# Kernel tuning notes

Measured on AMD Instinct MI355X. Metric: run time of the kernel, lower is better.

## Reference

```python
import jax, jax.numpy as jnp
import numpy as np

NUM_HEADS = 32
HEAD_DIM = 128
NUM_KV_HEADS = 8
SCALE = 0.08838834764831845  # 1/sqrt(128)
T = 2048          # total packed tokens (total_q == total_k in delta branch)
N_SAL = 512       # number of salient rows
NUM_SEQS = 4
EPS = 1e-8
NEG = -1e30


def setup_inputs() -> dict:
    key = jax.random.key(0)
    ks = jax.random.split(key, 5)
    q = jax.random.normal(ks[0], (T, NUM_HEADS, HEAD_DIM), dtype=jnp.float32)
    k = jax.random.normal(ks[1], (T, NUM_KV_HEADS, HEAD_DIM), dtype=jnp.float32)
    v = jax.random.normal(ks[2], (N_SAL, NUM_KV_HEADS, HEAD_DIM), dtype=jnp.float32)
    v_cache = jax.random.normal(ks[3], (T, NUM_KV_HEADS, HEAD_DIM), dtype=jnp.float32)
    c_cache = jax.random.normal(ks[4], (T, NUM_HEADS * HEAD_DIM), dtype=jnp.float32)
    # unique, sorted salient row indices (torch index_copy requires well-defined scatter)
    idx_salient_row = (jnp.arange(N_SAL, dtype=jnp.int64) * (T // N_SAL))
    # 4 equal packed sequences
    cu_seqlens = jnp.array([0, 512, 1024, 1536, 2048], dtype=jnp.int64)
    return {"q": q, "k": k, "v": v, "v_cache": v_cache, "c_cache": c_cache,
            "idx_salient_row": idx_salient_row, "cu_seqlens": cu_seqlens}


def _segment_ids(cu_seqlens, n):
    # seg[i] = which packed sequence row i belongs to (searchsorted right on bounds)
    return jnp.searchsorted(cu_seqlens[1:], jnp.arange(n), side="right")


def _sdpa(q_, k_, v_, seg_q_, seg_k_):
    # GQA: repeat_interleave kv heads to match query heads
    n_rep = q_.shape[1] // k_.shape[1]
    if n_rep > 1:
        k_ = jnp.repeat(k_, n_rep, axis=1)
        v_ = jnp.repeat(v_, n_rep, axis=1)
    scores = jnp.einsum("qhd,khd->hqk", q_, k_) * SCALE  # [H, nq, T]
    allow = (seg_q_[:, None] == seg_k_[None, :])          # [nq, T]
    scores = jnp.where(allow[None, :, :], scores, NEG)
    p = jax.nn.softmax(scores, axis=-1)
    return jnp.einsum("hqk,khd->qhd", p, v_)              # [nq, H, D]


def reference(q, k, v, v_cache, c_cache, idx_salient_row, cu_seqlens):
    total = q.shape[0]
    seg = _segment_ids(cu_seqlens, total)  # seg_q == seg_k (total_q == total_k)

    # delta KV-cache update at salient rows
    v_delta = v - v_cache[idx_salient_row]                      # [n_sal, Hkv, D]
    v_delta_sparse = jnp.zeros_like(k).at[idx_salient_row].set(v_delta)
    v_cache_new = v_cache.at[idx_salient_row].set(v)

    # salient-row full attention against updated cache
    o_salient = _sdpa(q[idx_salient_row], k, v_cache_new, seg[idx_salient_row], seg)
    # sparse delta attention for every row
    delta_c = _sdpa(q, k, v_delta_sparse, seg, seg)

    new_c_flat = c_cache + delta_c.reshape(total, -1)
    new_c_flat = new_c_flat.at[idx_salient_row].set(o_salient.reshape(o_salient.shape[0], -1))

    # cosine similarity between old and new context (early-exit signal)
    num = jnp.sum(c_cache * new_c_flat, axis=-1)
    den_c = jnp.sum(c_cache * c_cache, axis=-1)
    den_n = jnp.sum(new_c_flat * new_c_flat, axis=-1)
    cos_sim = num / (jnp.sqrt(den_c) * jnp.sqrt(den_n) + EPS)

    return new_c_flat.reshape(total, NUM_HEADS, HEAD_DIM), cos_sim
```

## Files before the change

### kernel.cpp

```cpp
#include <hip/hip_runtime.h>
#include <math.h>

#define NUM_HEADS 32
#define HEAD_DIM 128
#define NUM_KV_HEADS 8
#define SCALE 0.08838834764831845f
#define EPS 1e-8f
#define QT 32
#define BLK 512
#define SEGC_MAX 16
#define PD_CHUNKS 4
#define SAL_PAD 576
#define TLD 130

typedef __bf16 bf16x8 __attribute__((ext_vector_type(8)));
typedef float  f32x4  __attribute__((ext_vector_type(4)));

__device__ __forceinline__ float wave_sum(float v) {
#pragma unroll
    for (int o = 32; o > 0; o >>= 1) v += __shfl_down(v, o, 64);
    return v;
}


__global__ void setup_inv(int* inv, const int* idx, int T, int n_sal) {
    for (int i = threadIdx.x; i < T; i += blockDim.x) inv[i] = -1;
    __syncthreads();
    for (int s = threadIdx.x; s < n_sal; s += blockDim.x) inv[idx[s]] = s;
}

__global__ void conv_bf16(const float* __restrict__ src, __bf16* __restrict__ dst, int n8) {
    int i = blockIdx.x * blockDim.x + threadIdx.x;
    if (i < n8) {
        const float4* s4 = (const float4*)(src + (size_t)i * 8);
        float4 a = s4[0], b = s4[1];
        bf16x8 o;
        o[0]=(__bf16)a.x; o[1]=(__bf16)a.y; o[2]=(__bf16)a.z; o[3]=(__bf16)a.w;
        o[4]=(__bf16)b.x; o[5]=(__bf16)b.y; o[6]=(__bf16)b.z; o[7]=(__bf16)b.w;
        *(bf16x8*)(dst + (size_t)i * 8) = o;
    }
}

__global__ void build_vnewT(const float* __restrict__ v, const float* __restrict__ vc,
                            const int* __restrict__ inv, __bf16* __restrict__ vt,
                            int T, int Tpad) {
    const int kv = blockIdx.y;
    const int r0 = blockIdx.x * 64;
    __shared__ __bf16 tile[64 * TLD];
    for (int ii = threadIdx.x; ii < 64 * 32; ii += 256) {
        int r = ii >> 5, c4 = ii & 31;
        int row = r0 + r;
        float4 f = {0.f, 0.f, 0.f, 0.f};
        if (row < T) {
            int s2 = inv[row];
            const float* src = (s2 >= 0)
                ? v  + ((size_t)s2  * NUM_KV_HEADS + kv) * HEAD_DIM
                : vc + ((size_t)row * NUM_KV_HEADS + kv) * HEAD_DIM;
            f = *(const float4*)(src + c4 * 4);
        }
        __bf16* tp = &tile[r * TLD + c4 * 4];
        tp[0] = (__bf16)f.x; tp[1] = (__bf16)f.y; tp[2] = (__bf16)f.z; tp[3] = (__bf16)f.w;
    }
    __syncthreads();
    for (int ii = threadIdx.x; ii < 128 * 8; ii += 256) {
        int d = ii >> 3, rg = ii & 7;
        int row_out = r0 + rg * 8;
        if (row_out < Tpad) {
            bf16x8 o;
#pragma unroll
            for (int j = 0; j < 8; j++) o[j] = tile[(rg * 8 + j) * TLD + d];
            *(bf16x8*)(vt + ((size_t)kv * HEAD_DIM + d) * Tpad + row_out) = o;
        }
    }
}

__global__ void build_vdT(const float* __restrict__ v, const float* __restrict__ vc,
                          const int* __restrict__ idx, __bf16* __restrict__ vdt, int n_sal) {
    const int kv = blockIdx.y;
    const int s0 = blockIdx.x * 64;
    __shared__ __bf16 tile[64 * TLD];
    for (int ii = threadIdx.x; ii < 64 * 32; ii += 256) {
        int r = ii >> 5, c4 = ii & 31;
        int s = s0 + r;
        float4 f = {0.f, 0.f, 0.f, 0.f};
        if (s < n_sal) {
            int row = idx[s];
            float4 a = *(const float4*)(v  + ((size_t)s   * NUM_KV_HEADS + kv) * HEAD_DIM + c4 * 4);
            float4 b = *(const float4*)(vc + ((size_t)row * NUM_KV_HEADS + kv) * HEAD_DIM + c4 * 4);
            f.x = a.x - b.x; f.y = a.y - b.y; f.z = a.z - b.z; f.w = a.w - b.w;
        }
        __bf16* tp = &tile[r * TLD + c4 * 4];
        tp[0] = (__bf16)f.x; tp[1] = (__bf16)f.y; tp[2] = (__bf16)f.z; tp[3] = (__bf16)f.w;
    }
    __syncthreads();
    for (int ii = threadIdx.x; ii < 128 * 8; ii += 256) {
        int d = ii >> 3, rg = ii & 7;
        bf16x8 o;
#pragma unroll
        for (int j = 0; j < 8; j++) o[j] = tile[(rg * 8 + j) * TLD + d];
        *(bf16x8*)(vdt + ((size_t)kv * HEAD_DIM + d) * SAL_PAD + s0 + rg * 8) = o;
    }
}

__global__ __launch_bounds__(BLK, 4)
void attn_mfma(const float* __restrict__ q, const __bf16* __restrict__ kb,
               const __bf16* __restrict__ vnewT, const __bf16* __restrict__ vdT,
               const float* __restrict__ c_cache, const int* __restrict__ cu,
               const int* __restrict__ inv, const int* __restrict__ idx,
               float* __restrict__ out_c, int T, int Tpad, int n_seq, int n_sal) {
    const int qt    = blockIdx.x;
    const int h     = blockIdx.y;
    const int kvh   = h >> 2;
    const int qrow0 = qt * QT;
    const int tid   = threadIdx.x;
    const int wave  = tid >> 6;
    const int lane  = tid & 63;
    const int lm    = lane & 15;
    const int quad  = lane >> 4;

    __shared__ __align__(16) __bf16 Pb[SEGC_MAX * QT * 32];
    __shared__ __align__(16) __bf16 Pd[PD_CHUNKS * QT * 32];
    __shared__ int   scol[512];
    __shared__ float wred[8 * QT];
    __shared__ float linv[QT];
    __shared__ int   salrow[QT];
    __shared__ int   seginfo[4];

    if (tid == 0) {
        int seg_start = 0, seg_end = T;
        for (int s = 0; s < n_seq; s++) {
            int a = cu[s], b = cu[s + 1];
            if (qrow0 >= a && qrow0 < b) { seg_start = a; seg_end = b; }
        }
        int lo = 0, hi = n_sal;
        while (lo < hi) { int mid = (lo + hi) >> 1; if (idx[mid] < seg_start) lo = mid + 1; else hi = mid; }
        int slo = lo;
        hi = n_sal;
        while (lo < hi) { int mid = (lo + hi) >> 1; if (idx[mid] < seg_end) lo = mid + 1; else hi = mid; }
        seginfo[0] = seg_start; seginfo[1] = seg_end - seg_start;
        seginfo[2] = slo;       seginfo[3] = lo - slo;
    }
    if (tid < QT) salrow[tid] = inv[qrow0 + tid];
    __syncthreads();
    const int seg_start = seginfo[0], seg_len = seginfo[1];
    const int s_lo = seginfo[2], nss = seginfo[3];
    const int ntiles = (seg_len + 15) >> 4;
    const int SEGC   = (seg_len + 31) >> 5;

    for (int s = tid; s < nss; s += BLK) scol[s] = idx[s_lo + s] - seg_start;
    if (ntiles & 1) {
        for (int ii = tid; ii < QT * 16; ii += BLK) {
            int row = ii >> 4, col = ntiles * 16 + (ii & 15);
            Pb[((col >> 5) * QT + row) * 32 + (col & 31)] = (__bf16)0.f;
        }
    }

    bf16x8 aq[2][4];
#pragma unroll
    for (int rt = 0; rt < 2; rt++) {
        const float* qp = q + ((size_t)(qrow0 + rt * 16 + lm) * NUM_HEADS + h) * HEAD_DIM + quad * 8;
#pragma unroll
        for (int cc = 0; cc < 4; cc++) {
            float4 f0 = *(const float4*)(qp + cc * 32);
            float4 f1 = *(const float4*)(qp + cc * 32 + 4);
            bf16x8 a;
            a[0]=(__bf16)f0.x; a[1]=(__bf16)f0.y; a[2]=(__bf16)f0.z; a[3]=(__bf16)f0.w;
            a[4]=(__bf16)f1.x; a[5]=(__bf16)f1.y; a[6]=(__bf16)f1.z; a[7]=(__bf16)f1.w;
            aq[rt][cc] = a;
        }
    }

    float ps[2][4] = {{0.f,0.f,0.f,0.f},{0.f,0.f,0.f,0.f}};
#pragma unroll
    for (int tt = 0; tt < 4; tt++) {
        const int t = wave * 4 + tt;
        if (t < ntiles) {
            int key = seg_start + t * 16 + lm;
            if (key >= seg_start + seg_len) key = seg_start + seg_len - 1;
            const __bf16* kp = kb + ((size_t)key * NUM_KV_HEADS + kvh) * HEAD_DIM + quad * 8;
            bf16x8 b[4];
#pragma unroll
            for (int cc = 0; cc < 4; cc++) b[cc] = *(const bf16x8*)(kp + cc * 32);
            f32x4 acc[2] = {{0.f,0.f,0.f,0.f},{0.f,0.f,0.f,0.f}};
#pragma unroll
            for (int cc = 0; cc < 4; cc++) {
                acc[0] = __builtin_amdgcn_mfma_f32_16x16x32_bf16(aq[0][cc], b[cc], acc[0], 0, 0, 0);
                acc[1] = __builtin_amdgcn_mfma_f32_16x16x32_bf16(aq[1][cc], b[cc], acc[1], 0, 0, 0);
            }
            const int cc2 = t >> 1;
            const int j2  = (t & 1) * 16 + lm;
            const bool valid = (t * 16 + lm) < seg_len;
#pragma unroll
            for (int rt = 0; rt < 2; rt++) {
#pragma unroll
                for (int r = 0; r < 4; r++) {
                    float e = valid ? __expf(acc[rt][r] * SCALE) : 0.f;
                    ps[rt][r] += e;
                    const int row = rt * 16 + quad * 4 + r;
                    Pb[(cc2 * QT + row) * 32 + j2] = (__bf16)e;
                }
            }
        }
    }
#pragma unroll
    for (int rt = 0; rt < 2; rt++)
#pragma unroll
        for (int r = 0; r < 4; r++) {
#pragma unroll
            for (int msk = 1; msk <= 8; msk <<= 1)
                ps[rt][r] += __shfl_xor(ps[rt][r], msk, 64);
        }
    if (lm == 0) {
#pragma unroll
        for (int rt = 0; rt < 2; rt++)
#pragma unroll
            for (int r = 0; r < 4; r++)
                wred[wave * QT + rt * 16 + quad * 4 + r] = ps[rt][r];
    }
    __syncthreads();
    if (tid < QT) {
        float s = 0.f;
#pragma unroll
        for (int w = 0; w < 8; w++) s += wred[w * QT + tid];
        linv[tid] = 1.f / s;
    }

    const int dim = wave * 16 + lm;
    f32x4 accA[2] = {{0.f,0.f,0.f,0.f},{0.f,0.f,0.f,0.f}};
    f32x4 accB[2] = {{0.f,0.f,0.f,0.f},{0.f,0.f,0.f,0.f}};
    f32x4 accD[2] = {{0.f,0.f,0.f,0.f},{0.f,0.f,0.f,0.f}};
    const __bf16* vbase = vnewT + ((size_t)(kvh * HEAD_DIM) + wave * 16 + lm) * Tpad + seg_start;
    for (int cc = 0; cc < SEGC; cc++) {
        bf16x8 a0 = *(const bf16x8*)&Pb[(cc * QT +      lm) * 32 + quad * 8];
        bf16x8 a1 = *(const bf16x8*)&Pb[(cc * QT + 16 + lm) * 32 + quad * 8];
        bf16x8 bv = *(const bf16x8*)(vbase + cc * 32 + quad * 8);
        if (cc & 1) {
            accB[0] = __builtin_amdgcn_mfma_f32_16x16x32_bf16(a0, bv, accB[0], 0, 0, 0);
            accB[1] = __builtin_amdgcn_mfma_f32_16x16x32_bf16(a1, bv, accB[1], 0, 0, 0);
        } else {
            accA[0] = __builtin_amdgcn_mfma_f32_16x16x32_bf16(a0, bv, accA[0], 0, 0, 0);
            accA[1] = __builtin_amdgcn_mfma_f32_16x16x32_bf16(a1, bv, accA[1], 0, 0, 0);
        }
    }
    accA[0] += accB[0];
    accA[1] += accB[1];

    const int ndc = (nss + 31) >> 5;
    const bool al8 = ((s_lo & 7) == 0);
    for (int base = 0; base < ndc; base += PD_CHUNKS) {
        const int bc = min(PD_CHUNKS, ndc - base);
        __syncthreads();
        for (int ii = tid; ii < QT * (PD_CHUNKS * 32); ii += BLK) {
            int row = ii >> 7, srel = ii & 127;
            if (srel < bc * 32) {
                int s = base * 32 + srel;
                __bf16 e = (__bf16)0.f;
                if (s < nss) {
                    int col = scol[s];
                    e = Pb[((col >> 5) * QT + row) * 32 + (col & 31)];
                }
                Pd[((srel >> 5) * QT + row) * 32 + (srel & 31)] = e;
            }
        }
        __syncthreads();
        for (int dc = 0; dc < bc; dc++) {
            bf16x8 a0 = *(const bf16x8*)&Pd[(dc * QT +      lm) * 32 + quad * 8];
            bf16x8 a1 = *(const bf16x8*)&Pd[(dc * QT + 16 + lm) * 32 + quad * 8];
            const __bf16* vp = vdT + ((size_t)(kvh * HEAD_DIM) + wave * 16 + lm) * SAL_PAD
                             + s_lo + base * 32 + dc * 32 + quad * 8;
            bf16x8 bv;
            if (al8) bv = *(const bf16x8*)vp;
            else {
#pragma unroll
                for (int j = 0; j < 8; j++) bv[j] = vp[j];
            }
            accD[0] = __builtin_amdgcn_mfma_f32_16x16x32_bf16(a0, bv, accD[0], 0, 0, 0);
            accD[1] = __builtin_amdgcn_mfma_f32_16x16x32_bf16(a1, bv, accD[1], 0, 0, 0);
        }
    }
    __syncthreads();

#pragma unroll
    for (int rt = 0; rt < 2; rt++) {
#pragma unroll
        for (int r = 0; r < 4; r++) {
            const int row  = rt * 16 + quad * 4 + r;
            const int qrow = qrow0 + row;
            const float li = linv[row];
            float o;
            if (salrow[row] >= 0) {
                o = accA[rt][r] * li;
            } else {
                o = c_cache[(size_t)qrow * (NUM_HEADS * HEAD_DIM) + h * HEAD_DIM + dim]
                  + accD[rt][r] * li;
            }
            out_c[((size_t)qrow * NUM_HEADS + h) * HEAD_DIM + dim] = o;
        }
    }
}

__global__ void cos_kernel(const float* __restrict__ c_cache, const float* __restrict__ new_c,
                           float* __restrict__ out_cos, int T) {
    const int i = blockIdx.x;
    const int tid = threadIdx.x;
    const int CD = NUM_HEADS * HEAD_DIM;
    const float4* a = (const float4*)(c_cache + (size_t)i * CD);
    const float4* b = (const float4*)(new_c + (size_t)i * CD);
    float num = 0.f, dc = 0.f, dn = 0.f;
    for (int t = tid; t < CD / 4; t += blockDim.x) {
        float4 x = a[t], y = b[t];
        num = fmaf(x.x, y.x, fmaf(x.y, y.y, fmaf(x.z, y.z, fmaf(x.w, y.w, num))));
        dc  = fmaf(x.x, x.x, fmaf(x.y, x.y, fmaf(x.z, x.z, fmaf(x.w, x.w, dc))));
        dn  = fmaf(y.x, y.x, fmaf(y.y, y.y, fmaf(y.z, y.z, fmaf(y.w, y.w, dn))));
    }
    __shared__ float r0[4], r1[4], r2[4];
    num = wave_sum(num); dc = wave_sum(dc); dn = wave_sum(dn);
    int w = tid >> 6;
    if ((tid & 63) == 0) { r0[w] = num; r1[w] = dc; r2[w] = dn; }
    __syncthreads();
    if (tid == 0) {
        float n2 = r0[0] + r0[1] + r0[2] + r0[3];
        float c2 = r1[0] + r1[1] + r1[2] + r1[3];
        float d2 = r2[0] + r2[1] + r2[2] + r2[3];
        out_cos[i] = n2 / (sqrtf(c2) * sqrtf(d2) + EPS);
    }
}

extern "C" void kernel_launch(void* const* d_in, const int* in_sizes, int n_in,
                              void* d_out, int out_size, void* d_ws, size_t ws_size,
                              hipStream_t stream) {
    const float* q       = (const float*)d_in[0];
    const float* k       = (const float*)d_in[1];
    const float* v       = (const float*)d_in[2];
    const float* v_cache = (const float*)d_in[3];
    const float* c_cache = (const float*)d_in[4];
    const int*   idx     = (const int*)d_in[5];
    const int*   cu      = (const int*)d_in[6];

    const int T     = in_sizes[0] / (NUM_HEADS * HEAD_DIM);
    const int n_sal = in_sizes[5];
    const int n_seq = in_sizes[6] - 1;
    const int Tpad  = T + 32;

    float* out_c   = (float*)d_out;
    float* out_cos = out_c + (size_t)T * NUM_HEADS * HEAD_DIM;

    char* wsp = (char*)d_ws;
    size_t off = 0;
    int* inv = (int*)(wsp + off);
    off += ((size_t)T * sizeof(int) + 255) & ~(size_t)255;
    __bf16* kb = (__bf16*)(wsp + off);
    off += (((size_t)T * NUM_KV_HEADS * HEAD_DIM * 2) + 255) & ~(size_t)255;
    __bf16* vnewT = (__bf16*)(wsp + off);
    off += (((size_t)NUM_KV_HEADS * HEAD_DIM * Tpad * 2) + 255) & ~(size_t)255;
    __bf16* vdT = (__bf16*)(wsp + off);
    off += ((size_t)NUM_KV_HEADS * HEAD_DIM * SAL_PAD * 2 + 255) & ~(size_t)255;
    (void)ws_size;

    setup_inv<<<1, 256, 0, stream>>>(inv, idx, T, n_sal);

    int n8k = T * NUM_KV_HEADS * HEAD_DIM / 8;
    conv_bf16<<<(n8k + 255) / 256, 256, 0, stream>>>(k, kb, n8k);

    dim3 gvt((Tpad + 63) / 64, NUM_KV_HEADS);
    build_vnewT<<<gvt, 256, 0, stream>>>(v, v_cache, inv, vnewT, T, Tpad);
    dim3 gvd(SAL_PAD / 64, NUM_KV_HEADS);
    build_vdT<<<gvd, 256, 0, stream>>>(v, v_cache, idx, vdT, n_sal);

    dim3 grid(T / QT, NUM_HEADS);
    attn_mfma<<<grid, BLK, 0, stream>>>(q, kb, vnewT, vdT, c_cache, cu, inv, idx,
                                        out_c, T, Tpad, n_seq, n_sal);

    cos_kernel<<<T, 256, 0, stream>>>(c_cache, out_c, out_cos, T);
}
```

Before: 251.0 us.

## Fuse prep kernels, fold cosine partials into attention, restructure P layout

Merges the K conversion, V-new transpose and V-delta transpose into one prep launch and drops the inverse-index setup kernel in favour of binary searches. The attention kernel now prefetches old context values, computes per-head cosine partial sums in its epilogue, and a small finalize kernel reduces them, so the separate full re-read of c_cache and out_c is gone. The QK MFMA operands are swapped so probabilities are stored row-major with a padded stride, and the PV loop is fully unrolled for full-length segments. This cuts launches and memory traffic but adds a partial-sum buffer and more per-block epilogue shuffles.

```diff
diff --git a/kernel.cpp b/kernel.cpp
--- a/kernel.cpp
+++ b/kernel.cpp
@@ -6,99 +6,113 @@
 #define NUM_KV_HEADS 8
 #define SCALE 0.08838834764831845f
 #define EPS 1e-8f
+#define MAX_SEG 512
 #define QT 32
 #define BLK 512
 #define SEGC_MAX 16
 #define PD_CHUNKS 4
 #define SAL_PAD 576
+#define PB_STRIDE 520
+#define PD_STRIDE 136
 #define TLD 130
+#define CD (NUM_HEADS * HEAD_DIM)
 
 typedef __bf16 bf16x8 __attribute__((ext_vector_type(8)));
+typedef __bf16 bf16x4 __attribute__((ext_vector_type(4)));
 typedef float  f32x4  __attribute__((ext_vector_type(4)));
 
-__device__ __forceinline__ float wave_sum(float v) {
-#pragma unroll
-    for (int o = 32; o > 0; o >>= 1) v += __shfl_down(v, o, 64);
-    return v;
-}
-
-
-__global__ void setup_inv(int* inv, const int* idx, int T, int n_sal) {
-    for (int i = threadIdx.x; i < T; i += blockDim.x) inv[i] = -1;
-    __syncthreads();
-    for (int s = threadIdx.x; s < n_sal; s += blockDim.x) inv[idx[s]] = s;
-}
-
-__global__ void conv_bf16(const float* __restrict__ src, __bf16* __restrict__ dst, int n8) {
-    int i = blockIdx.x * blockDim.x + threadIdx.x;
-    if (i < n8) {
-        const float4* s4 = (const float4*)(src + (size_t)i * 8);
-        float4 a = s4[0], b = s4[1];
-        bf16x8 o;
-        o[0]=(__bf16)a.x; o[1]=(__bf16)a.y; o[2]=(__bf16)a.z; o[3]=(__bf16)a.w;
-        o[4]=(__bf16)b.x; o[5]=(__bf16)b.y; o[6]=(__bf16)b.z; o[7]=(__bf16)b.w;
-        *(bf16x8*)(dst + (size_t)i * 8) = o;
-    }
-}
-
-__global__ void build_vnewT(const float* __restrict__ v, const float* __restrict__ vc,
-                            const int* __restrict__ inv, __bf16* __restrict__ vt,
-                            int T, int Tpad) {
-    const int kv = blockIdx.y;
-    const int r0 = blockIdx.x * 64;
+__device__ __forceinline__ int lower_bound_i(const int* __restrict__ a, int n, int key) {
+    int lo = 0, hi = n;
+    while (lo < hi) { int mid = (lo + hi) >> 1; if (a[mid] < key) lo = mid + 1; else hi = mid; }
+    return lo;
+}
+__device__ __forceinline__ int bsearch_eq(const int* __restrict__ a, int n, int key) {
+    int lo = lower_bound_i(a, n, key);
+    return (lo < n && a[lo] == key) ? lo : -1;
+}
+
+__global__ void prep(const float* __restrict__ k, const float* __restrict__ v,
+                     const float* __restrict__ vc, const int* __restrict__ idx,
+                     __bf16* __restrict__ kb, __bf16* __restrict__ vnewT,
+                     __bf16* __restrict__ vdT, int T, int Tpad, int n_sal,
+                     int nb_conv, int nb_vt) {
     __shared__ __bf16 tile[64 * TLD];
-    for (int ii = threadIdx.x; ii < 64 * 32; ii += 256) {
-        int r = ii >> 5, c4 = ii & 31;
-        int row = r0 + r;
-        float4 f = {0.f, 0.f, 0.f, 0.f};
-        if (row < T) {
-            int s2 = inv[row];
-            const float* src = (s2 >= 0)
-                ? v  + ((size_t)s2  * NUM_KV_HEADS + kv) * HEAD_DIM
-                : vc + ((size_t)row * NUM_KV_HEADS + kv) * HEAD_DIM;
-            f = *(const float4*)(src + c4 * 4);
-        }
-        __bf16* tp = &tile[r * TLD + c4 * 4];
-        tp[0] = (__bf16)f.x; tp[1] = (__bf16)f.y; tp[2] = (__bf16)f.z; tp[3] = (__bf16)f.w;
-    }
-    __syncthreads();
-    for (int ii = threadIdx.x; ii < 128 * 8; ii += 256) {
-        int d = ii >> 3, rg = ii & 7;
-        int row_out = r0 + rg * 8;
-        if (row_out < Tpad) {
+    __shared__ int sal_of[64];
+    const int b = blockIdx.x;
+    const int tid = threadIdx.x;
+
+    if (b < nb_conv) {
+        int i = b * 256 + tid;
+        int n8 = T * NUM_KV_HEADS * HEAD_DIM / 8;
+        if (i < n8) {
+            const float4* s4 = (const float4*)(k + (size_t)i * 8);
+            float4 a = s4[0], bb = s4[1];
             bf16x8 o;
+            o[0]=(__bf16)a.x; o[1]=(__bf16)a.y; o[2]=(__bf16)a.z; o[3]=(__bf16)a.w;
+            o[4]=(__bf16)bb.x; o[5]=(__bf16)bb.y; o[6]=(__bf16)bb.z; o[7]=(__bf16)bb.w;
+            *(bf16x8*)(kb + (size_t)i * 8) = o;
+        }
+        return;
+    }
+    if (b < nb_conv + nb_vt * NUM_KV_HEADS) {
+        const int bb = b - nb_conv;
+        const int kv = bb / nb_vt;
+        const int r0 = (bb % nb_vt) * 64;
+        if (tid < 64) sal_of[tid] = bsearch_eq(idx, n_sal, r0 + tid);
+        __syncthreads();
+        for (int ii = tid; ii < 64 * 32; ii += 256) {
+            int r = ii >> 5, c4 = ii & 31;
+            int row = r0 + r;
+            float4 f = {0.f, 0.f, 0.f, 0.f};
+            if (row < T) {
+                int s2 = sal_of[r];
+                const float* src = (s2 >= 0)
+                    ? v  + ((size_t)s2  * NUM_KV_HEADS + kv) * HEAD_DIM
+                    : vc + ((size_t)row * NUM_KV_HEADS + kv) * HEAD_DIM;
+                f = *(const float4*)(src + c4 * 4);
+            }
+            __bf16* tp = &tile[r * TLD + c4 * 4];
+            tp[0] = (__bf16)f.x; tp[1] = (__bf16)f.y; tp[2] = (__bf16)f.z; tp[3] = (__bf16)f.w;
+        }
+        __syncthreads();
+        for (int ii = tid; ii < 128 * 8; ii += 256) {
+            int d = ii >> 3, rg = ii & 7;
+            int row_out = r0 + rg * 8;
+            if (row_out < Tpad) {
+                bf16x8 o;
+#pragma unroll
+                for (int j = 0; j < 8; j++) o[j] = tile[(rg * 8 + j) * TLD + d];
+                *(bf16x8*)(vnewT + ((size_t)kv * HEAD_DIM + d) * Tpad + row_out) = o;
+            }
+        }
+        return;
+    }
+    {
+        const int bb = b - nb_conv - nb_vt * NUM_KV_HEADS;
+        const int nvd = SAL_PAD / 64;
+        const int kv = bb / nvd;
+        const int s0 = (bb % nvd) * 64;
+        for (int ii = tid; ii < 64 * 32; ii += 256) {
+            int r = ii >> 5, c4 = ii & 31;
+            int s = s0 + r;
+            float4 f = {0.f, 0.f, 0.f, 0.f};
+            if (s < n_sal) {
+                int row = idx[s];
+                float4 a = *(const float4*)(v  + ((size_t)s   * NUM_KV_HEADS + kv) * HEAD_DIM + c4 * 4);
+                float4 bb2 = *(const float4*)(vc + ((size_t)row * NUM_KV_HEADS + kv) * HEAD_DIM + c4 * 4);
+                f.x = a.x - bb2.x; f.y = a.y - bb2.y; f.z = a.z - bb2.z; f.w = a.w - bb2.w;
+            }
+            __bf16* tp = &tile[r * TLD + c4 * 4];
+            tp[0] = (__bf16)f.x; tp[1] = (__bf16)f.y; tp[2] = (__bf16)f.z; tp[3] = (__bf16)f.w;
+        }
+        __syncthreads();
+        for (int ii = tid; ii < 128 * 8; ii += 256) {
+            int d = ii >> 3, rg = ii & 7;
+            bf16x8 o;
 #pragma unroll
             for (int j = 0; j < 8; j++) o[j] = tile[(rg * 8 + j) * TLD + d];
-            *(bf16x8*)(vt + ((size_t)kv * HEAD_DIM + d) * Tpad + row_out) = o;
-        }
-    }
-}
-
-__global__ void build_vdT(const float* __restrict__ v, const float* __restrict__ vc,
-                          const int* __restrict__ idx, __bf16* __restrict__ vdt, int n_sal) {
-    const int kv = blockIdx.y;
-    const int s0 = blockIdx.x * 64;
-    __shared__ __bf16 tile[64 * TLD];
-    for (int ii = threadIdx.x; ii < 64 * 32; ii += 256) {
-        int r = ii >> 5, c4 = ii & 31;
-        int s = s0 + r;
-        float4 f = {0.f, 0.f, 0.f, 0.f};
-        if (s < n_sal) {
-            int row = idx[s];
-            float4 a = *(const float4*)(v  + ((size_t)s   * NUM_KV_HEADS + kv) * HEAD_DIM + c4 * 4);
-            float4 b = *(const float4*)(vc + ((size_t)row * NUM_KV_HEADS + kv) * HEAD_DIM + c4 * 4);
-            f.x = a.x - b.x; f.y = a.y - b.y; f.z = a.z - b.z; f.w = a.w - b.w;
-        }
-        __bf16* tp = &tile[r * TLD + c4 * 4];
-        tp[0] = (__bf16)f.x; tp[1] = (__bf16)f.y; tp[2] = (__bf16)f.z; tp[3] = (__bf16)f.w;
-    }
-    __syncthreads();
-    for (int ii = threadIdx.x; ii < 128 * 8; ii += 256) {
-        int d = ii >> 3, rg = ii & 7;
-        bf16x8 o;
-#pragma unroll
-        for (int j = 0; j < 8; j++) o[j] = tile[(rg * 8 + j) * TLD + d];
-        *(bf16x8*)(vdt + ((size_t)kv * HEAD_DIM + d) * SAL_PAD + s0 + rg * 8) = o;
+            *(bf16x8*)(vdT + ((size_t)kv * HEAD_DIM + d) * SAL_PAD + s0 + rg * 8) = o;
+        }
     }
 }
 
@@ -106,8 +120,8 @@
 void attn_mfma(const float* __restrict__ q, const __bf16* __restrict__ kb,
                const __bf16* __restrict__ vnewT, const __bf16* __restrict__ vdT,
                const float* __restrict__ c_cache, const int* __restrict__ cu,
-               const int* __restrict__ inv, const int* __restrict__ idx,
-               float* __restrict__ out_c, int T, int Tpad, int n_seq, int n_sal) {
+               const int* __restrict__ idx, float* __restrict__ out_c,
+               float* __restrict__ cospart, int T, int Tpad, int n_seq, int n_sal) {
     const int qt    = blockIdx.x;
     const int h     = blockIdx.y;
     const int kvh   = h >> 2;
@@ -118,40 +132,41 @@
     const int lm    = lane & 15;
     const int quad  = lane >> 4;
 
-    __shared__ __align__(16) __bf16 Pb[SEGC_MAX * QT * 32];
-    __shared__ __align__(16) __bf16 Pd[PD_CHUNKS * QT * 32];
-    __shared__ int   scol[512];
+    __shared__ __align__(16) __bf16 Pb[QT * PB_STRIDE];
+    __shared__ __align__(16) __bf16 Pd[QT * PD_STRIDE];
+    __shared__ int   scol[MAX_SEG];
     __shared__ float wred[8 * QT];
     __shared__ float linv[QT];
     __shared__ int   salrow[QT];
-    __shared__ int   seginfo[4];
-
-    if (tid == 0) {
-        int seg_start = 0, seg_end = T;
-        for (int s = 0; s < n_seq; s++) {
-            int a = cu[s], b = cu[s + 1];
-            if (qrow0 >= a && qrow0 < b) { seg_start = a; seg_end = b; }
-        }
-        int lo = 0, hi = n_sal;
-        while (lo < hi) { int mid = (lo + hi) >> 1; if (idx[mid] < seg_start) lo = mid + 1; else hi = mid; }
-        int slo = lo;
-        hi = n_sal;
-        while (lo < hi) { int mid = (lo + hi) >> 1; if (idx[mid] < seg_end) lo = mid + 1; else hi = mid; }
-        seginfo[0] = seg_start; seginfo[1] = seg_end - seg_start;
-        seginfo[2] = slo;       seginfo[3] = lo - slo;
-    }
-    if (tid < QT) salrow[tid] = inv[qrow0 + tid];
-    __syncthreads();
-    const int seg_start = seginfo[0], seg_len = seginfo[1];
-    const int s_lo = seginfo[2], nss = seginfo[3];
+
+    int seg_start = 0, seg_end = T;
+    for (int s = 0; s < n_seq; s++) {
+        int a = cu[s], bnd = cu[s + 1];
+        if (qrow0 >= a && qrow0 < bnd) { seg_start = a; seg_end = bnd; }
+    }
+    const int seg_len = seg_end - seg_start;
+    const int s_lo = lower_bound_i(idx, n_sal, seg_start);
+    const int s_hi = lower_bound_i(idx, n_sal, seg_end);
+    const int nss  = s_hi - s_lo;
     const int ntiles = (seg_len + 15) >> 4;
     const int SEGC   = (seg_len + 31) >> 5;
 
+    const int dim = wave * 16 + lm;
+
+    const float* cbase = c_cache + (size_t)qrow0 * CD + h * HEAD_DIM + dim;
+    float cold[2][4];
+#pragma unroll
+    for (int rt = 0; rt < 2; rt++)
+#pragma unroll
+        for (int r = 0; r < 4; r++)
+            cold[rt][r] = cbase[(size_t)(rt * 16 + quad * 4 + r) * CD];
+
+    if (tid < QT) salrow[tid] = bsearch_eq(idx, n_sal, qrow0 + tid);
     for (int s = tid; s < nss; s += BLK) scol[s] = idx[s_lo + s] - seg_start;
-    if (ntiles & 1) {
+    if (ntiles * 16 < SEGC * 32) {
         for (int ii = tid; ii < QT * 16; ii += BLK) {
             int row = ii >> 4, col = ntiles * 16 + (ii & 15);
-            Pb[((col >> 5) * QT + row) * 32 + (col & 31)] = (__bf16)0.f;
+            Pb[row * PB_STRIDE + col] = (__bf16)0.f;
         }
     }
 
@@ -170,7 +185,7 @@
         }
     }
 
-    float ps[2][4] = {{0.f,0.f,0.f,0.f},{0.f,0.f,0.f,0.f}};
+    float ps[2] = {0.f, 0.f};
 #pragma unroll
     for (int tt = 0; tt < 4; tt++) {
         const int t = wave * 4 + tt;
@@ -178,44 +193,37 @@
             int key = seg_start + t * 16 + lm;
             if (key >= seg_start + seg_len) key = seg_start + seg_len - 1;
             const __bf16* kp = kb + ((size_t)key * NUM_KV_HEADS + kvh) * HEAD_DIM + quad * 8;
-            bf16x8 b[4];
-#pragma unroll
-            for (int cc = 0; cc < 4; cc++) b[cc] = *(const bf16x8*)(kp + cc * 32);
+            bf16x8 bk[4];
+#pragma unroll
+            for (int cc = 0; cc < 4; cc++) bk[cc] = *(const bf16x8*)(kp + cc * 32);
             f32x4 acc[2] = {{0.f,0.f,0.f,0.f},{0.f,0.f,0.f,0.f}};
 #pragma unroll
             for (int cc = 0; cc < 4; cc++) {
-                acc[0] = __builtin_amdgcn_mfma_f32_16x16x32_bf16(aq[0][cc], b[cc], acc[0], 0, 0, 0);
-                acc[1] = __builtin_amdgcn_mfma_f32_16x16x32_bf16(aq[1][cc], b[cc], acc[1], 0, 0, 0);
-            }
-            const int cc2 = t >> 1;
-            const int j2  = (t & 1) * 16 + lm;
-            const bool valid = (t * 16 + lm) < seg_len;
+                acc[0] = __builtin_amdgcn_mfma_f32_16x16x32_bf16(bk[cc], aq[0][cc], acc[0], 0, 0, 0);
+                acc[1] = __builtin_amdgcn_mfma_f32_16x16x32_bf16(bk[cc], aq[1][cc], acc[1], 0, 0, 0);
+            }
 #pragma unroll
             for (int rt = 0; rt < 2; rt++) {
+                bf16x4 pk;
 #pragma unroll
                 for (int r = 0; r < 4; r++) {
-                    float e = valid ? __expf(acc[rt][r] * SCALE) : 0.f;
-                    ps[rt][r] += e;
-                    const int row = rt * 16 + quad * 4 + r;
-                    Pb[(cc2 * QT + row) * 32 + j2] = (__bf16)e;
+                    const int kl = t * 16 + quad * 4 + r;
+                    float e = (kl < seg_len) ? __expf(acc[rt][r] * SCALE) : 0.f;
+                    ps[rt] += e;
+                    pk[r] = (__bf16)e;
                 }
-            }
-        }
-    }
-#pragma unroll
-    for (int rt = 0; rt < 2; rt++)
-#pragma unroll
-        for (int r = 0; r < 4; r++) {
-#pragma unroll
-            for (int msk = 1; msk <= 8; msk <<= 1)
-                ps[rt][r] += __shfl_xor(ps[rt][r], msk, 64);
-        }
-    if (lm == 0) {
-#pragma unroll
-        for (int rt = 0; rt < 2; rt++)
-#pragma unroll
-            for (int r = 0; r < 4; r++)
-                wred[wave * QT + rt * 16 + quad * 4 + r] = ps[rt][r];
+                *(bf16x4*)&Pb[(rt * 16 + lm) * PB_STRIDE + t * 16 + quad * 4] = pk;
+            }
+        }
+    }
+#pragma unroll
+    for (int m = 16; m <= 32; m <<= 1) {
+        ps[0] += __shfl_xor(ps[0], m, 64);
+        ps[1] += __shfl_xor(ps[1], m, 64);
+    }
+    if (quad == 0) {
+        wred[wave * QT + lm]      = ps[0];
+        wred[wave * QT + 16 + lm] = ps[1];
     }
     __syncthreads();
     if (tid < QT) {
@@ -225,104 +233,115 @@
         linv[tid] = 1.f / s;
     }
 
-    const int dim = wave * 16 + lm;
-    f32x4 accA[2] = {{0.f,0.f,0.f,0.f},{0.f,0.f,0.f,0.f}};
-    f32x4 accB[2] = {{0.f,0.f,0.f,0.f},{0.f,0.f,0.f,0.f}};
+    f32x4 acc0a = {0.f,0.f,0.f,0.f}, acc0b = {0.f,0.f,0.f,0.f};
+    f32x4 acc1a = {0.f,0.f,0.f,0.f}, acc1b = {0.f,0.f,0.f,0.f};
+    const __bf16* vbase = vnewT + ((size_t)kvh * HEAD_DIM + dim) * Tpad + seg_start + quad * 8;
+    const __bf16* pb0 = &Pb[lm * PB_STRIDE + quad * 8];
+    const __bf16* pb1 = &Pb[(16 + lm) * PB_STRIDE + quad * 8];
+
+#define PV_BODY(cc)  {                                                              \
+        bf16x8 a0 = *(const bf16x8*)(pb0 + (cc) * 32);                              \
+        bf16x8 a1 = *(const bf16x8*)(pb1 + (cc) * 32);                              \
+        bf16x8 bv = *(const bf16x8*)(vbase + (cc) * 32);                            \
+        if ((cc) & 1) {                                                             \
+            acc0b = __builtin_amdgcn_mfma_f32_16x16x32_bf16(a0, bv, acc0b, 0, 0, 0);\
+            acc1b = __builtin_amdgcn_mfma_f32_16x16x32_bf16(a1, bv, acc1b, 0, 0, 0);\
+        } else {                                                                    \
+            acc0a = __builtin_amdgcn_mfma_f32_16x16x32_bf16(a0, bv, acc0a, 0, 0, 0);\
+            acc1a = __builtin_amdgcn_mfma_f32_16x16x32_bf16(a1, bv, acc1a, 0, 0, 0);\
+        } }
+
+    if (SEGC == SEGC_MAX) {
+#pragma unroll
+        for (int cc = 0; cc < SEGC_MAX; cc++) PV_BODY(cc)
+    } else {
+        for (int cc = 0; cc < SEGC; cc++) PV_BODY(cc)
+    }
+    f32x4 accF[2];
+    accF[0] = acc0a + acc0b;
+    accF[1] = acc1a + acc1b;
+
     f32x4 accD[2] = {{0.f,0.f,0.f,0.f},{0.f,0.f,0.f,0.f}};
-    const __bf16* vbase = vnewT + ((size_t)(kvh * HEAD_DIM) + wave * 16 + lm) * Tpad + seg_start;
-    for (int cc = 0; cc < SEGC; cc++) {
-        bf16x8 a0 = *(const bf16x8*)&Pb[(cc * QT +      lm) * 32 + quad * 8];
-        bf16x8 a1 = *(const bf16x8*)&Pb[(cc * QT + 16 + lm) * 32 + quad * 8];
-        bf16x8 bv = *(const bf16x8*)(vbase + cc * 32 + quad * 8);
-        if (cc & 1) {
-            accB[0] = __builtin_amdgcn_mfma_f32_16x16x32_bf16(a0, bv, accB[0], 0, 0, 0);
-            accB[1] = __builtin_amdgcn_mfma_f32_16x16x32_bf16(a1, bv, accB[1], 0, 0, 0);
-        } else {
-            accA[0] = __builtin_amdgcn_mfma_f32_16x16x32_bf16(a0, bv, accA[0], 0, 0, 0);
-            accA[1] = __builtin_amdgcn_mfma_f32_16x16x32_bf16(a1, bv, accA[1], 0, 0, 0);
-        }
-    }
-    accA[0] += accB[0];
-    accA[1] += accB[1];
-
     const int ndc = (nss + 31) >> 5;
     const bool al8 = ((s_lo & 7) == 0);
+    const __bf16* vdbase = vdT + ((size_t)kvh * HEAD_DIM + dim) * SAL_PAD + s_lo + quad * 8;
     for (int base = 0; base < ndc; base += PD_CHUNKS) {
         const int bc = min(PD_CHUNKS, ndc - base);
         __syncthreads();
-        for (int ii = tid; ii < QT * (PD_CHUNKS * 32); ii += BLK) {
+        for (int ii = tid; ii < QT * PD_CHUNKS * 32; ii += BLK) {
             int row = ii >> 7, srel = ii & 127;
-            if (srel < bc * 32) {
-                int s = base * 32 + srel;
-                __bf16 e = (__bf16)0.f;
-                if (s < nss) {
-                    int col = scol[s];
-                    e = Pb[((col >> 5) * QT + row) * 32 + (col & 31)];
+            int s = base * 32 + srel;
+            __bf16 e = (__bf16)0.f;
+            if (srel < bc * 32 && s < nss) e = Pb[row * PB_STRIDE + scol[s]];
+            Pd[row * PD_STRIDE + srel] = e;
+        }
+        __syncthreads();
+#pragma unroll
+        for (int dc = 0; dc < PD_CHUNKS; dc++) {
+            if (dc < bc) {
+                bf16x8 a0 = *(const bf16x8*)&Pd[lm * PD_STRIDE + dc * 32 + quad * 8];
+                bf16x8 a1 = *(const bf16x8*)&Pd[(16 + lm) * PD_STRIDE + dc * 32 + quad * 8];
+                const __bf16* vp = vdbase + (base + dc) * 32;
+                bf16x8 bv;
+                if (al8) bv = *(const bf16x8*)vp;
+                else {
+#pragma unroll
+                    for (int j = 0; j < 8; j++) bv[j] = vp[j];
                 }
-                Pd[((srel >> 5) * QT + row) * 32 + (srel & 31)] = e;
-            }
-        }
-        __syncthreads();
-        for (int dc = 0; dc < bc; dc++) {
-            bf16x8 a0 = *(const bf16x8*)&Pd[(dc * QT +      lm) * 32 + quad * 8];
-            bf16x8 a1 = *(const bf16x8*)&Pd[(dc * QT + 16 + lm) * 32 + quad * 8];
-            const __bf16* vp = vdT + ((size_t)(kvh * HEAD_DIM) + wave * 16 + lm) * SAL_PAD
-                             + s_lo + base * 32 + dc * 32 + quad * 8;
-            bf16x8 bv;
-            if (al8) bv = *(const bf16x8*)vp;
-            else {
-#pragma unroll
-                for (int j = 0; j < 8; j++) bv[j] = vp[j];
-            }
-            accD[0] = __builtin_amdgcn_mfma_f32_16x16x32_bf16(a0, bv, accD[0], 0, 0, 0);
-            accD[1] = __builtin_amdgcn_mfma_f32_16x16x32_bf16(a1, bv, accD[1], 0, 0, 0);
+                accD[0] = __builtin_amdgcn_mfma_f32_16x16x32_bf16(a0, bv, accD[0], 0, 0, 0);
+                accD[1] = __builtin_amdgcn_mfma_f32_16x16x32_bf16(a1, bv, accD[1], 0, 0, 0);
+            }
         }
     }
     __syncthreads();
 
+    float* cp = (float*)Pd;
+    float* obase = out_c + (size_t)qrow0 * CD + h * HEAD_DIM + dim;
 #pragma unroll
     for (int rt = 0; rt < 2; rt++) {
 #pragma unroll
         for (int r = 0; r < 4; r++) {
-            const int row  = rt * 16 + quad * 4 + r;
-            const int qrow = qrow0 + row;
+            const int row = rt * 16 + quad * 4 + r;
+            const float c_old = cold[rt][r];
             const float li = linv[row];
             float o;
-            if (salrow[row] >= 0) {
-                o = accA[rt][r] * li;
-            } else {
-                o = c_cache[(size_t)qrow * (NUM_HEADS * HEAD_DIM) + h * HEAD_DIM + dim]
-                  + accD[rt][r] * li;
-            }
-            out_c[((size_t)qrow * NUM_HEADS + h) * HEAD_DIM + dim] = o;
-        }
-    }
-}
-
-__global__ void cos_kernel(const float* __restrict__ c_cache, const float* __restrict__ new_c,
-                           float* __restrict__ out_cos, int T) {
-    const int i = blockIdx.x;
-    const int tid = threadIdx.x;
-    const int CD = NUM_HEADS * HEAD_DIM;
-    const float4* a = (const float4*)(c_cache + (size_t)i * CD);
-    const float4* b = (const float4*)(new_c + (size_t)i * CD);
-    float num = 0.f, dc = 0.f, dn = 0.f;
-    for (int t = tid; t < CD / 4; t += blockDim.x) {
-        float4 x = a[t], y = b[t];
-        num = fmaf(x.x, y.x, fmaf(x.y, y.y, fmaf(x.z, y.z, fmaf(x.w, y.w, num))));
-        dc  = fmaf(x.x, x.x, fmaf(x.y, x.y, fmaf(x.z, x.z, fmaf(x.w, x.w, dc))));
-        dn  = fmaf(y.x, y.x, fmaf(y.y, y.y, fmaf(y.z, y.z, fmaf(y.w, y.w, dn))));
-    }
-    __shared__ float r0[4], r1[4], r2[4];
-    num = wave_sum(num); dc = wave_sum(dc); dn = wave_sum(dn);
-    int w = tid >> 6;
-    if ((tid & 63) == 0) { r0[w] = num; r1[w] = dc; r2[w] = dn; }
+            if (salrow[row] >= 0) o = accF[rt][r] * li;
+            else                  o = c_old + accD[rt][r] * li;
+            obase[(size_t)row * CD] = o;
+            float xn = o * c_old, xc = c_old * c_old, xd = o * o;
+#pragma unroll
+            for (int m = 1; m <= 8; m <<= 1) {
+                xn += __shfl_xor(xn, m, 64);
+                xc += __shfl_xor(xc, m, 64);
+                xd += __shfl_xor(xd, m, 64);
+            }
+            if (lm == 0) {
+                cp[(wave * 3 + 0) * QT + row] = xn;
+                cp[(wave * 3 + 1) * QT + row] = xc;
+                cp[(wave * 3 + 2) * QT + row] = xd;
+            }
+        }
+    }
     __syncthreads();
-    if (tid == 0) {
-        float n2 = r0[0] + r0[1] + r0[2] + r0[3];
-        float c2 = r1[0] + r1[1] + r1[2] + r1[3];
-        float d2 = r2[0] + r2[1] + r2[2] + r2[3];
-        out_cos[i] = n2 / (sqrtf(c2) * sqrtf(d2) + EPS);
+    for (int ii = tid; ii < 3 * QT; ii += BLK) {
+        int c = ii >> 5, row = ii & 31;
+        float s = 0.f;
+#pragma unroll
+        for (int w = 0; w < 8; w++) s += cp[(w * 3 + c) * QT + row];
+        cospart[((size_t)(qrow0 + row) * NUM_HEADS + h) * 3 + c] = s;
+    }
+}
+
+__global__ void cos_finalize(const float* __restrict__ cospart, float* __restrict__ out_cos, int T) {
+    int i = blockIdx.x * blockDim.x + threadIdx.x;
+    if (i < T) {
+        const float* p = cospart + (size_t)i * NUM_HEADS * 3;
+        float n = 0.f, c = 0.f, d = 0.f;
+#pragma unroll
+        for (int h2 = 0; h2 < NUM_HEADS; h2++) {
+            n += p[h2 * 3 + 0]; c += p[h2 * 3 + 1]; d += p[h2 * 3 + 2];
+        }
+        out_cos[i] = n / (sqrtf(c) * sqrtf(d) + EPS);
     }
 }
 
@@ -337,39 +356,37 @@
     const int*   idx     = (const int*)d_in[5];
     const int*   cu      = (const int*)d_in[6];
 
-    const int T     = in_sizes[0] / (NUM_HEADS * HEAD_DIM);
+    const int T     = in_sizes[0] / CD;
     const int n_sal = in_sizes[5];
     const int n_seq = in_sizes[6] - 1;
     const int Tpad  = T + 32;
 
     float* out_c   = (float*)d_out;
-    float* out_cos = out_c + (size_t)T * NUM_HEADS * HEAD_DIM;
+    float* out_cos = out_c + (size_t)T * CD;
 
     char* wsp = (char*)d_ws;
     size_t off = 0;
-    int* inv = (int*)(wsp + off);
-    off += ((size_t)T * sizeof(int) + 255) & ~(size_t)255;
     __bf16* kb = (__bf16*)(wsp + off);
     off += (((size_t)T * NUM_KV_HEADS * HEAD_DIM * 2) + 255) & ~(size_t)255;
     __bf16* vnewT = (__bf16*)(wsp + off);
     off += (((size_t)NUM_KV_HEADS * HEAD_DIM * Tpad * 2) + 255) & ~(size_t)255;
     __bf16* vdT = (__bf16*)(wsp + off);
     off += ((size_t)NUM_KV_HEADS * HEAD_DIM * SAL_PAD * 2 + 255) & ~(size_t)255;
+    float* cospart = (float*)(wsp + off);
+    off += ((size_t)T * NUM_HEADS * 3 * 4 + 255) & ~(size_t)255;
     (void)ws_size;
 
-    setup_inv<<<1, 256, 0, stream>>>(inv, idx, T, n_sal);
-
-    int n8k = T * NUM_KV_HEADS * HEAD_DIM / 8;
-    conv_bf16<<<(n8k + 255) / 256, 256, 0, stream>>>(k, kb, n8k);
-
-    dim3 gvt((Tpad + 63) / 64, NUM_KV_HEADS);
-    build_vnewT<<<gvt, 256, 0, stream>>>(v, v_cache, inv, vnewT, T, Tpad);
-    dim3 gvd(SAL_PAD / 64, NUM_KV_HEADS);
-    build_vdT<<<gvd, 256, 0, stream>>>(v, v_cache, idx, vdT, n_sal);
+    const int nb_conv = (T * NUM_KV_HEADS * HEAD_DIM / 8 + 255) / 256;
+    const int nb_vt   = (Tpad + 63) / 64;
+    const int nb_vd   = SAL_PAD / 64;
+    const int nb_tot  = nb_conv + nb_vt * NUM_KV_HEADS + nb_vd * NUM_KV_HEADS;
+
+    prep<<<nb_tot, 256, 0, stream>>>(k, v, v_cache, idx, kb, vnewT, vdT,
+                                     T, Tpad, n_sal, nb_conv, nb_vt);
 
     dim3 grid(T / QT, NUM_HEADS);
-    attn_mfma<<<grid, BLK, 0, stream>>>(q, kb, vnewT, vdT, c_cache, cu, inv, idx,
-                                        out_c, T, Tpad, n_seq, n_sal);
-
-    cos_kernel<<<T, 256, 0, stream>>>(c_cache, out_c, out_cos, T);
-}
+    attn_mfma<<<grid, BLK, 0, stream>>>(q, kb, vnewT, vdT, c_cache, cu, idx,
+                                        out_c, cospart, T, Tpad, n_seq, n_sal);
+
+    cos_finalize<<<(T + 255) / 256, 256, 0, stream>>>(cospart, out_cos, T);
+}
```

Result: faster. 240.9 us (-4.0%).
